# Optimization experiments

Hardware: AMD Instinct MI355X
Metric: run time of the kernel (lower is better)

## Reference

```python
import jax, jax.numpy as jnp
import numpy as np

GX = GY = GZ = 128
VOXEL_DIM = 28  # 1 density + 27 SH coefficients (9 per RGB channel)
NUM_RAYS = 8192
NUM_SAMPLES = 128


def sh_basis(theta, phi):
    """Degree-2 SH basis in the coefficient order used by harmonic():
    [Y_0_0, Y_m1_1, Y_0_1, Y_1_1, Y_m2_2, Y_m1_2, Y_0_2, Y_1_2, Y_2_2]."""
    y00 = 0.5 * jnp.sqrt(1.0 / jnp.pi)
    h3 = 0.5 * jnp.sqrt(3.0 / jnp.pi)
    q5 = 0.25 * jnp.sqrt(5.0 / jnp.pi)
    h15 = 0.5 * jnp.sqrt(15.0 / jnp.pi)
    q15 = 0.25 * jnp.sqrt(15.0 / jnp.pi)
    st, ct = jnp.sin(theta), jnp.cos(theta)
    sp, cp = jnp.sin(phi), jnp.cos(phi)
    return jnp.stack([
        y00 * jnp.ones_like(theta),          # Y_0_0
        h3 * st * sp,                        # Y_m1_1
        h3 * ct,                             # Y_0_1
        h3 * st * cp,                        # Y_1_1
        h15 * st * cp * st * sp,             # Y_m2_2
        h15 * st * sp * ct,                  # Y_m1_2
        q5 * (3.0 * ct * ct - 1.0),          # Y_0_2
        h15 * st * cp * ct,                  # Y_1_2
        q15 * ((st * cp) ** 2 - (st * sp) ** 2),  # Y_2_2
    ])


def trilinear(grid, pos):
    """grid: [GX,GY,GZ,D]; pos: [R,S,3] -> [R,S,D] interpolated features."""
    p0 = jnp.floor(pos).astype(jnp.int32)
    fr = pos - p0.astype(pos.dtype)
    x0, y0, z0 = p0[..., 0], p0[..., 1], p0[..., 2]
    xd, yd, zd = fr[..., 0:1], fr[..., 1:2], fr[..., 2:3]
    c000 = grid[x0, y0, z0]
    c001 = grid[x0, y0, z0 + 1]
    c010 = grid[x0, y0 + 1, z0]
    c011 = grid[x0, y0 + 1, z0 + 1]
    c100 = grid[x0 + 1, y0, z0]
    c101 = grid[x0 + 1, y0, z0 + 1]
    c110 = grid[x0 + 1, y0 + 1, z0]
    c111 = grid[x0 + 1, y0 + 1, z0 + 1]
    c00 = c000 * (1 - xd) + c100 * xd
    c01 = c001 * (1 - xd) + c101 * xd
    c10 = c010 * (1 - xd) + c110 * xd
    c11 = c011 * (1 - xd) + c111 * xd
    c0 = c00 * (1 - yd) + c10 * yd
    c1 = c01 * (1 - yd) + c11 * yd
    return c0 * (1 - zd) + c1 * zd


def setup_inputs() -> dict:
    key = jax.random.key(0)
    k1, k2, k3, k4 = jax.random.split(key, 4)
    voxel_grid = jax.random.uniform(k1, (GX, GY, GZ, VOXEL_DIM), dtype=jnp.float32)
    # sample positions inside [0, G-2] so the +1 corner stays in bounds
    sample_positions = jax.random.uniform(
        k2, (NUM_RAYS, NUM_SAMPLES, 3), dtype=jnp.float32) * (GX - 2)
    sample_distances = jax.random.uniform(
        k3, (NUM_RAYS, NUM_SAMPLES), dtype=jnp.float32) * 0.1
    viewing_angle = jax.random.uniform(k4, (2,), dtype=jnp.float32) * np.pi
    return {
        "voxel_grid": voxel_grid,
        "sample_positions": sample_positions,
        "sample_distances": sample_distances,
        "viewing_angle": viewing_angle,
    }


def reference(voxel_grid, sample_positions, sample_distances, viewing_angle):
    R, S = sample_distances.shape
    feats = trilinear(voxel_grid, sample_positions)          # [R,S,28]
    sigma = feats[..., 0]                                     # [R,S]
    sh_coeffs = feats[..., 1:].reshape(R, S, 3, 9)            # [R,S,3,9]
    basis = sh_basis(viewing_angle[0], viewing_angle[1])      # [9]
    rgb = jnp.einsum('rsck,k->rsc', sh_coeffs, basis)         # [R,S,3]
    tau = sigma * sample_distances                            # [R,S]
    att = jnp.exp(-tau)
    # faithful to channel_opacity_z: transmittance is the CUMULATIVE SUM of
    # exp(-sigma_j * d_j) over j = 0..k (inclusive of current sample)
    transmittance = jnp.cumsum(att, axis=1)
    alpha = 1.0 - att
    weights = transmittance * alpha                           # [R,S]
    return jnp.sum(weights[..., None] * rgb, axis=1)          # [R,3]
```

## Files before the change

### kernel.cpp

```cpp
#include <hip/hip_runtime.h>
#include <hip/hip_fp16.h>
#include <math.h>

#define GXD 128
#define GYD 128
#define GZD 128
#define VD 28
#define NRAYS 8192
#define NSAMP 128
#define NVOX (GXD * GYD * GZD)

__global__ __launch_bounds__(256) void predot_quad(
    const float* __restrict__ g,
    const float* __restrict__ ang,
    uint2* __restrict__ o)
{
    __shared__ float sb[9];
    if (threadIdx.x == 0) {
        float st, ct, sp, cp;
        sincosf(ang[0], &st, &ct);
        sincosf(ang[1], &sp, &cp);
        sb[0] = 0.28209479177387814f;
        sb[1] = 0.4886025119029199f * st * sp;
        sb[2] = 0.4886025119029199f * ct;
        sb[3] = 0.4886025119029199f * st * cp;
        sb[4] = 1.0925484305920792f * st * cp * st * sp;
        sb[5] = 1.0925484305920792f * st * sp * ct;
        sb[6] = 0.31539156525252005f * (3.0f * ct * ct - 1.0f);
        sb[7] = 1.0925484305920792f * st * cp * ct;
        sb[8] = 0.5462742152960396f * ((st * cp) * (st * cp) - (st * sp) * (st * sp));
    }
    __syncthreads();

    const int xhi = blockIdx.x >> 6;
    const int yhi = blockIdx.x & 63;
    const int obase = blockIdx.x << 9;

    #pragma unroll
    for (int q = 0; q < 2; ++q) {
        const int w   = q * 256 + threadIdx.x;
        const int col = w >> 7;
        const int z   = w & 127;
        const int x   = (xhi << 1) + (col >> 1);
        const int y   = (yhi << 1) + (col & 1);
        const size_t v = (((size_t)x << 7) | y) << 7 | z;

        const float4* __restrict__ p = (const float4*)(g + v * VD);
        float f[28];
        #pragma unroll
        for (int i = 0; i < 7; ++i)
            ((float4*)f)[i] = p[i];

        float r = 0.0f, gg = 0.0f, b = 0.0f;
        #pragma unroll
        for (int k = 0; k < 9; ++k) {
            r  += sb[k] * f[1 + k];
            gg += sb[k] * f[10 + k];
            b  += sb[k] * f[19 + k];
        }
        const __half2 h0 = __floats2half2_rn(f[0], r);
        const __half2 h1 = __floats2half2_rn(gg, b);
        uint2 u;
        u.x = *(const unsigned*)&h0;
        u.y = *(const unsigned*)&h1;
        o[obase + (z << 2) + col] = u;
    }
}

#define LERP4(a, b, t) make_float4( \
    fmaf((t), (b).x - (a).x, (a).x), \
    fmaf((t), (b).y - (a).y, (a).y), \
    fmaf((t), (b).z - (a).z, (a).z), \
    fmaf((t), (b).w - (a).w, (a).w))

__device__ __forceinline__ float4 fetch_q(const uint2* __restrict__ vg,
                                          int x, int y, int z)
{
    const int p   = ((x >> 1) << 6) | (y >> 1);
    const int col = ((x & 1) << 1) | (y & 1);
    const uint2 u = vg[(p << 9) | (z << 2) | col];
    const float2 sr = __half22float2(*(const __half2*)&u.x);
    const float2 gb = __half22float2(*(const __half2*)&u.y);
    return make_float4(sr.x, sr.y, gb.x, gb.y);
}

__global__ __launch_bounds__(256) void render_q(
    const uint2* __restrict__ vg,
    const float* __restrict__ pos,
    const float* __restrict__ dist,
    float* __restrict__ out)
{
    __shared__ float4 srgb[2][NSAMP];

    const int tid  = threadIdx.x;
    const int rloc = tid >> 7;
    const int s    = tid & 127;
    const int ray  = blockIdx.x * 2 + rloc;
    const int sidx = ray * NSAMP + s;

    const float px = pos[sidx * 3 + 0];
    const float py = pos[sidx * 3 + 1];
    const float pz = pos[sidx * 3 + 2];
    const int ix = (int)floorf(px);
    const int iy = (int)floorf(py);
    const int iz = (int)floorf(pz);
    const float fx = px - (float)ix;
    const float fy = py - (float)iy;
    const float fz = pz - (float)iz;

    const float4 c000 = fetch_q(vg, ix,     iy,     iz);
    const float4 c001 = fetch_q(vg, ix,     iy,     iz + 1);
    const float4 c010 = fetch_q(vg, ix,     iy + 1, iz);
    const float4 c011 = fetch_q(vg, ix,     iy + 1, iz + 1);
    const float4 c100 = fetch_q(vg, ix + 1, iy,     iz);
    const float4 c101 = fetch_q(vg, ix + 1, iy,     iz + 1);
    const float4 c110 = fetch_q(vg, ix + 1, iy + 1, iz);
    const float4 c111 = fetch_q(vg, ix + 1, iy + 1, iz + 1);

    const float4 a00 = LERP4(c000, c001, fz);
    const float4 a01 = LERP4(c010, c011, fz);
    const float4 a10 = LERP4(c100, c101, fz);
    const float4 a11 = LERP4(c110, c111, fz);
    const float4 a0  = LERP4(a00, a01, fy);
    const float4 a1  = LERP4(a10, a11, fy);
    const float4 a   = LERP4(a0, a1, fx);

    const float d   = dist[sidx];
    const float att = expf(-a.x * d);
    srgb[rloc][s] = make_float4(att, a.y, a.z, a.w);
    __syncthreads();

    if ((tid & 127) < 64) {
        const int lane = tid & 63;
        const float4 a0v = srgb[rloc][lane];
        const float4 a1v = srgb[rloc][lane + 64];
        const float att0 = a0v.x;
        const float att1 = a1v.x;

        float scan_lo = att0;
        #pragma unroll
        for (int off = 1; off < 64; off <<= 1) {
            const float v = __shfl_up(scan_lo, off, 64);
            if (lane >= off) scan_lo += v;
        }
        const float total_lo = __shfl(scan_lo, 63, 64);

        float scan_hi = att1;
        #pragma unroll
        for (int off = 1; off < 64; off <<= 1) {
            const float v = __shfl_up(scan_hi, off, 64);
            if (lane >= off) scan_hi += v;
        }
        const float w_lo = scan_lo * (1.0f - att0);
        const float w_hi = (total_lo + scan_hi) * (1.0f - att1);

        float o0 = w_lo * a0v.y + w_hi * a1v.y;
        float o1 = w_lo * a0v.z + w_hi * a1v.z;
        float o2 = w_lo * a0v.w + w_hi * a1v.w;

        #pragma unroll
        for (int off = 32; off > 0; off >>= 1) {
            o0 += __shfl_xor(o0, off, 64);
            o1 += __shfl_xor(o1, off, 64);
            o2 += __shfl_xor(o2, off, 64);
        }
        if (lane == 0) {
            out[ray * 3 + 0] = o0;
            out[ray * 3 + 1] = o1;
            out[ray * 3 + 2] = o2;
        }
    }
}

__global__ __launch_bounds__(1024) void plenoxel_fused32(
    const float* __restrict__ grid,
    const float* __restrict__ pos,
    const float* __restrict__ dist,
    const float* __restrict__ ang,
    float* __restrict__ out)
{
    __shared__ float4 srgb[NSAMP];
    const int ray  = blockIdx.x;
    const int tid  = threadIdx.x;
    const int s    = tid >> 3;
    const int subl = tid & 7;
    const int dx   = (subl >> 2) & 1;
    const int dy   = (subl >> 1) & 1;
    const int zh   = subl & 1;

    const float theta = ang[0], phi = ang[1];
    float st, ct, sp, cp;
    sincosf(theta, &st, &ct);
    sincosf(phi,   &sp, &cp);
    float basis[9];
    basis[0] = 0.28209479177387814f;
    basis[1] = 0.4886025119029199f * st * sp;
    basis[2] = 0.4886025119029199f * ct;
    basis[3] = 0.4886025119029199f * st * cp;
    basis[4] = 1.0925484305920792f * st * cp * st * sp;
    basis[5] = 1.0925484305920792f * st * sp * ct;
    basis[6] = 0.31539156525252005f * (3.0f * ct * ct - 1.0f);
    basis[7] = 1.0925484305920792f * st * cp * ct;
    basis[8] = 0.5462742152960396f * ((st * cp) * (st * cp) - (st * sp) * (st * sp));

    const int sidx = ray * NSAMP + s;
    const float px = pos[sidx * 3 + 0];
    const float py = pos[sidx * 3 + 1];
    const float pz = pos[sidx * 3 + 2];
    const int ix = (int)floorf(px);
    const int iy = (int)floorf(py);
    const int iz = (int)floorf(pz);
    const float fx = px - (float)ix;
    const float fy = py - (float)iy;
    const float fz = pz - (float)iz;

    const float w = (dx ? fx : 1.0f - fx) *
                    (dy ? fy : 1.0f - fy) *
                    (zh ? fz : 1.0f - fz);

    const int base = (((ix + dx) * GYD + (iy + dy)) * GZD + (iz + zh)) * VD;
    const float4* __restrict__ q = (const float4*)(grid + base);
    float f[28];
    #pragma unroll
    for (int i = 0; i < 7; ++i)
        ((float4*)f)[i] = q[i];

    float psig = w * f[0];
    float pr = 0.0f, pg = 0.0f, pb = 0.0f;
    #pragma unroll
    for (int k = 0; k < 9; ++k) {
        pr += basis[k] * f[1 + k];
        pg += basis[k] * f[10 + k];
        pb += basis[k] * f[19 + k];
    }
    pr *= w; pg *= w; pb *= w;

    #pragma unroll
    for (int off = 1; off < 8; off <<= 1) {
        psig += __shfl_xor(psig, off, 64);
        pr   += __shfl_xor(pr,   off, 64);
        pg   += __shfl_xor(pg,   off, 64);
        pb   += __shfl_xor(pb,   off, 64);
    }
    if (subl == 0) srgb[s] = make_float4(psig, pr, pg, pb);
    __syncthreads();

    if (tid < 64) {
        const int lane = tid;
        const float4 a0 = srgb[lane];
        const float4 a1 = srgb[lane + 64];
        const float d0 = dist[ray * NSAMP + lane];
        const float d1 = dist[ray * NSAMP + lane + 64];
        const float att0 = expf(-a0.x * d0);
        const float att1 = expf(-a1.x * d1);

        float scan_lo = att0;
        #pragma unroll
        for (int off = 1; off < 64; off <<= 1) {
            const float v = __shfl_up(scan_lo, off, 64);
            if (lane >= off) scan_lo += v;
        }
        const float total_lo = __shfl(scan_lo, 63, 64);
        float scan_hi = att1;
        #pragma unroll
        for (int off = 1; off < 64; off <<= 1) {
            const float v = __shfl_up(scan_hi, off, 64);
            if (lane >= off) scan_hi += v;
        }
        const float w_lo = scan_lo * (1.0f - att0);
        const float w_hi = (total_lo + scan_hi) * (1.0f - att1);

        float o0 = w_lo * a0.y + w_hi * a1.y;
        float o1 = w_lo * a0.z + w_hi * a1.z;
        float o2 = w_lo * a0.w + w_hi * a1.w;
        #pragma unroll
        for (int off = 32; off > 0; off >>= 1) {
            o0 += __shfl_xor(o0, off, 64);
            o1 += __shfl_xor(o1, off, 64);
            o2 += __shfl_xor(o2, off, 64);
        }
        if (lane == 0) {
            out[ray * 3 + 0] = o0;
            out[ray * 3 + 1] = o1;
            out[ray * 3 + 2] = o2;
        }
    }
}

extern "C" void kernel_launch(void* const* d_in, const int* in_sizes, int n_in,
                              void* d_out, int out_size, void* d_ws, size_t ws_size,
                              hipStream_t stream) {
    const float* grid = (const float*)d_in[0];
    const float* pos  = (const float*)d_in[1];
    const float* dist = (const float*)d_in[2];
    const float* ang  = (const float*)d_in[3];
    float* out = (float*)d_out;

    const size_t need = (size_t)NVOX * sizeof(uint2);
    if (ws_size >= need) {
        uint2* vg = (uint2*)d_ws;
        predot_quad<<<4096, 256, 0, stream>>>(grid, ang, vg);
        render_q<<<NRAYS / 2, 256, 0, stream>>>(vg, pos, dist, out);
    } else {
        plenoxel_fused32<<<NRAYS, 1024, 0, stream>>>(grid, pos, dist, ang, out);
    }
}
```

Baseline: 379.7 us.

## Duplicate z+1 neighbor into each packed voxel entry to halve gather count

The precompute kernel now writes a 16-byte entry per voxel holding both its own fp16 (sigma,r,g,b) and the values of the voxel at z+1, with z-major/column-minor ordering inside each 2x2 xy tile. The render kernel then does four 16-byte gathers with an in-register z-lerp instead of eight 8-byte gathers. This cuts the number of random memory transactions per sample, at the cost of doubling the intermediate buffer size and its write traffic. The z=127 slot's duplicate half is left unwritten, which is fine only because sample positions stay within bounds.

```diff
diff --git a/kernel.cpp b/kernel.cpp
--- a/kernel.cpp
+++ b/kernel.cpp
@@ -10,10 +10,10 @@
 #define NSAMP 128
 #define NVOX (GXD * GYD * GZD)
 
-__global__ __launch_bounds__(256) void predot_quad(
+__global__ __launch_bounds__(256) void predot_dupz(
     const float* __restrict__ g,
     const float* __restrict__ ang,
-    uint2* __restrict__ o)
+    char* __restrict__ o)
 {
     __shared__ float sb[9];
     if (threadIdx.x == 0) {
@@ -34,16 +34,16 @@
 
     const int xhi = blockIdx.x >> 6;
     const int yhi = blockIdx.x & 63;
-    const int obase = blockIdx.x << 9;
+    char* __restrict__ ob = o + (size_t)blockIdx.x * 8192;
 
     #pragma unroll
     for (int q = 0; q < 2; ++q) {
         const int w   = q * 256 + threadIdx.x;
-        const int col = w >> 7;
-        const int z   = w & 127;
+        const int z   = w >> 2;
+        const int col = w & 3;
         const int x   = (xhi << 1) + (col >> 1);
         const int y   = (yhi << 1) + (col & 1);
-        const size_t v = (((size_t)x << 7) | y) << 7 | z;
+        const size_t v = ((((size_t)x << 7) | y) << 7) | z;
 
         const float4* __restrict__ p = (const float4*)(g + v * VD);
         float f[28];
@@ -63,7 +63,10 @@
         uint2 u;
         u.x = *(const unsigned*)&h0;
         u.y = *(const unsigned*)&h1;
-        o[obase + (z << 2) + col] = u;
+
+        *(uint2*)(ob + w * 16) = u;
+        if (w >= 4)
+            *(uint2*)(ob + (w - 4) * 16 + 8) = u;
     }
 }
 
@@ -73,19 +76,24 @@
     fmaf((t), (b).z - (a).z, (a).z), \
     fmaf((t), (b).w - (a).w, (a).w))
 
-__device__ __forceinline__ float4 fetch_q(const uint2* __restrict__ vg,
-                                          int x, int y, int z)
+__device__ __forceinline__ float4 zlerp_fetch(const uint4* __restrict__ vg,
+                                              int x, int y, int z, float fz)
 {
     const int p   = ((x >> 1) << 6) | (y >> 1);
     const int col = ((x & 1) << 1) | (y & 1);
-    const uint2 u = vg[(p << 9) | (z << 2) | col];
-    const float2 sr = __half22float2(*(const __half2*)&u.x);
-    const float2 gb = __half22float2(*(const __half2*)&u.y);
-    return make_float4(sr.x, sr.y, gb.x, gb.y);
-}
-
-__global__ __launch_bounds__(256) void render_q(
-    const uint2* __restrict__ vg,
+    const uint4 u = vg[(p << 9) | (z << 2) | col];
+    const float2 aa = __half22float2(*(const __half2*)&u.x);
+    const float2 ab = __half22float2(*(const __half2*)&u.y);
+    const float2 ba = __half22float2(*(const __half2*)&u.z);
+    const float2 bb = __half22float2(*(const __half2*)&u.w);
+    return make_float4(fmaf(fz, ba.x - aa.x, aa.x),
+                       fmaf(fz, ba.y - aa.y, aa.y),
+                       fmaf(fz, bb.x - ab.x, ab.x),
+                       fmaf(fz, bb.y - ab.y, ab.y));
+}
+
+__global__ __launch_bounds__(256) void render_d(
+    const uint4* __restrict__ vg,
     const float* __restrict__ pos,
     const float* __restrict__ dist,
     float* __restrict__ out)
@@ -108,22 +116,14 @@
     const float fy = py - (float)iy;
     const float fz = pz - (float)iz;
 
-    const float4 c000 = fetch_q(vg, ix,     iy,     iz);
-    const float4 c001 = fetch_q(vg, ix,     iy,     iz + 1);
-    const float4 c010 = fetch_q(vg, ix,     iy + 1, iz);
-    const float4 c011 = fetch_q(vg, ix,     iy + 1, iz + 1);
-    const float4 c100 = fetch_q(vg, ix + 1, iy,     iz);
-    const float4 c101 = fetch_q(vg, ix + 1, iy,     iz + 1);
-    const float4 c110 = fetch_q(vg, ix + 1, iy + 1, iz);
-    const float4 c111 = fetch_q(vg, ix + 1, iy + 1, iz + 1);
-
-    const float4 a00 = LERP4(c000, c001, fz);
-    const float4 a01 = LERP4(c010, c011, fz);
-    const float4 a10 = LERP4(c100, c101, fz);
-    const float4 a11 = LERP4(c110, c111, fz);
-    const float4 a0  = LERP4(a00, a01, fy);
-    const float4 a1  = LERP4(a10, a11, fy);
-    const float4 a   = LERP4(a0, a1, fx);
+    const float4 a00 = zlerp_fetch(vg, ix,     iy,     iz, fz);
+    const float4 a01 = zlerp_fetch(vg, ix,     iy + 1, iz, fz);
+    const float4 a10 = zlerp_fetch(vg, ix + 1, iy,     iz, fz);
+    const float4 a11 = zlerp_fetch(vg, ix + 1, iy + 1, iz, fz);
+
+    const float4 a0 = LERP4(a00, a01, fy);
+    const float4 a1 = LERP4(a10, a11, fy);
+    const float4 a  = LERP4(a0, a1, fx);
 
     const float d   = dist[sidx];
     const float att = expf(-a.x * d);
@@ -296,11 +296,10 @@
     const float* ang  = (const float*)d_in[3];
     float* out = (float*)d_out;
 
-    const size_t need = (size_t)NVOX * sizeof(uint2);
+    const size_t need = (size_t)NVOX * 16;
     if (ws_size >= need) {
-        uint2* vg = (uint2*)d_ws;
-        predot_quad<<<4096, 256, 0, stream>>>(grid, ang, vg);
-        render_q<<<NRAYS / 2, 256, 0, stream>>>(vg, pos, dist, out);
+        predot_dupz<<<4096, 256, 0, stream>>>(grid, ang, (char*)d_ws);
+        render_d<<<NRAYS / 2, 256, 0, stream>>>((const uint4*)d_ws, pos, dist, out);
     } else {
         plenoxel_fused32<<<NRAYS, 1024, 0, stream>>>(grid, pos, dist, ang, out);
     }
```

After: 368.2 us. 3.0% less time.
